# Kernel tuning notes

Measured on AMD Instinct MI355X. Metric: run time of the kernel, lower is better.

## Reference

```python
import jax, jax.numpy as jnp
import numpy as np

N = 100000   # num_nodes
E = 1600000  # num_edges
R = 8        # num_rels
B = 4        # num_bases
D = 64       # inp_dim = h_dim = out_dim


def setup_inputs() -> dict:
    key = jax.random.key(0)
    ks = jax.random.split(key, 16)
    s = 1.0 / np.sqrt(D)
    inp = {
        'h': jax.random.normal(ks[0], (N, D), jnp.float32),
        'src': jax.random.randint(ks[1], (E,), 0, N),
        'dst': jax.random.randint(ks[2], (E,), 0, N),
        'etype': jax.random.randint(ks[3], (E,), 0, R),
        'norm': jax.random.uniform(ks[4], (E, 1), jnp.float32),
    }
    for i in range(3):  # i2h, hidden, h2o layers (basis decomposition)
        inp[f'bases{i}'] = jax.random.normal(ks[5 + 2 * i], (B, D, D), jnp.float32) * s
        inp[f'wcomp{i}'] = jax.random.normal(ks[6 + 2 * i], (R, B), jnp.float32) * s
    inp['dec_w1'] = jax.random.normal(ks[11], (D, D), jnp.float32) * s
    inp['dec_b1'] = jnp.zeros((D,), jnp.float32)
    inp['dec_w2'] = jax.random.normal(ks[12], (D, 1), jnp.float32) * s
    inp['dec_b2'] = jnp.zeros((1,), jnp.float32)
    return inp


def rgcn_layer(h, src, dst, etype, norm, bases, wcomp, activate):
    # basis decomposition: W_r = sum_b wcomp[r,b] * bases[b]
    W = jnp.einsum('rb,bio->rio', wcomp, bases)           # [R, D, D]
    # transform all nodes under every relation (dense GEMM), then gather per edge
    Ht = jnp.einsum('ni,rio->rno', h, W).reshape(R * N, -1)  # [R*N, D]
    msg = Ht[etype * N + src] * norm                      # [E, D] gather + norm
    out = jax.ops.segment_sum(msg, dst, num_segments=N)   # scatter-add to dst
    return jax.nn.relu(out) if activate else out


def reference(h, src, dst, etype, norm, bases0, wcomp0, bases1, wcomp1,
              bases2, wcomp2, dec_w1, dec_b1, dec_w2, dec_b2):
    # EncoderRGCN: i2h (relu) -> hidden (relu) -> h2o (no activation)
    h1 = rgcn_layer(h, src, dst, etype, norm, bases0, wcomp0, True)
    h2 = rgcn_layer(h1, src, dst, etype, norm, bases1, wcomp1, True)
    henc = rgcn_layer(h2, src, dst, etype, norm, bases2, wcomp2, False)
    # AttributeDecoder: Linear -> ReLU -> Linear(reconstruct_dim=1)
    d1 = jax.nn.relu(henc @ dec_w1 + dec_b1)
    rec = (d1 @ dec_w2 + dec_b2).squeeze()                # [N]
    return rec, henc
```

## Files before the change

kernel.cpp:

```cpp
#include <hip/hip_runtime.h>

typedef _Float16 half8 __attribute__((ext_vector_type(8)));
typedef _Float16 half4 __attribute__((ext_vector_type(4)));
typedef _Float16 half2v __attribute__((ext_vector_type(2)));
typedef float floatx4 __attribute__((ext_vector_type(4)));

constexpr int NN = 100000;
constexpr int EE = 1600000;
constexpr int NBK = 196;
constexpr int CHUNK = 3125;
constexpr int CAPB = 12288;
constexpr int NDCAP = 48;

__global__ __launch_bounds__(256) void k_part(const int* __restrict__ dst,
                                              const int* __restrict__ src,
                                              const int* __restrict__ etype,
                                              const float* __restrict__ norm,
                                              int* __restrict__ gcur,
                                              int2* __restrict__ part) {
  __shared__ int2 ldata[CHUNK];
  __shared__ unsigned char lbkt[CHUNK];
  __shared__ int lhist[NBK], lbase[NBK + 1], lcur[NBK], gbase[NBK];
  __shared__ int sh[256];
  const int tid = threadIdx.x;
  const int e0 = blockIdx.x * CHUNK;

  for (int b = tid; b < NBK; b += 256) lhist[b] = 0;
  __syncthreads();
  for (int i = tid; i < CHUNK; i += 256)
    atomicAdd(&lhist[dst[e0 + i] >> 9], 1);
  __syncthreads();
  {
    const int v = (tid < NBK) ? lhist[tid] : 0;
    sh[tid] = v;
    __syncthreads();
    int run = v;
    for (int d = 1; d < 256; d <<= 1) {
      int t = (tid >= d) ? sh[tid - d] : 0;
      __syncthreads();
      run += t;
      sh[tid] = run;
      __syncthreads();
    }
    if (tid < NBK) {
      lbase[tid] = run - v;
      lcur[tid] = 0;
      gbase[tid] = tid * CAPB + atomicAdd(&gcur[tid], v);
    }
    if (tid == 0) lbase[NBK] = CHUNK;
  }
  __syncthreads();
  for (int i = tid; i < CHUNK; i += 256) {
    const int e = e0 + i;
    const int d = dst[e], s = src[e], et = etype[e];
    const _Float16 nh = (_Float16)norm[e];
    const unsigned short n16 = __builtin_bit_cast(unsigned short, nh);
    const int bk = d >> 9;
    const int pos = lbase[bk] + atomicAdd(&lcur[bk], 1);
    ldata[pos] = make_int2((d << 15) | (s >> 2), (s & 3) | (et << 2) | ((int)n16 << 5));
    lbkt[pos] = (unsigned char)bk;
  }
  __syncthreads();
  for (int i = tid; i < CHUNK; i += 256) {
    const int bk = (int)lbkt[i];
    part[gbase[bk] + (i - lbase[bk])] = ldata[i];
  }
}

__global__ __launch_bounds__(512) void k_part2(const int* __restrict__ gcur,
                                               const int2* __restrict__ part,
                                               int* __restrict__ off,
                                               int2* __restrict__ em) {
  __shared__ int hcnt[512];
  __shared__ int wred[8];
  __shared__ int swsum[8];
  const int tid = threadIdx.x;
  const int bk = blockIdx.x;
  const int nb0 = bk << 9;
  const int2* __restrict__ pp = part + (size_t)bk * CAPB;

  {
    int pv = (tid < bk) ? gcur[tid] : 0;
    for (int d = 32; d > 0; d >>= 1) pv += __shfl_down(pv, d);
    if ((tid & 63) == 0) wred[tid >> 6] = pv;
  }
  hcnt[tid] = 0;
  __syncthreads();
  int base = 0;
#pragma unroll
  for (int w = 0; w < 8; ++w) base += wred[w];
  const int cntb = gcur[bk];

  for (int i = tid; i < cntb; i += 512)
    atomicAdd(&hcnt[(((unsigned)pp[i].x) >> 15) & 511], 1);
  __syncthreads();
  const int v = hcnt[tid];
  int incl = v;
  for (int d = 1; d < 64; d <<= 1) {
    const int t = __shfl_up(incl, d);
    if ((tid & 63) >= d) incl += t;
  }
  if ((tid & 63) == 63) swsum[tid >> 6] = incl;
  __syncthreads();
  int pre = 0;
  for (int w = 0; w < (tid >> 6); ++w) pre += swsum[w];
  const int excl = pre + incl - v;
  {
    const int n = nb0 + tid;
    if (n < NN) off[n] = base + excl;
  }
  if (bk == NBK - 1 && tid == 0) off[NN] = EE;
  hcnt[tid] = excl;
  __syncthreads();
  for (int i = tid; i < cntb; i += 512) {
    const int2 r = pp[i];
    const int d = ((unsigned)r.x) >> 15;
    const int s = ((r.x & 0x7FFF) << 2) | (r.y & 3);
    const int et = (r.y >> 2) & 7;
    const unsigned short n16 = (unsigned short)((r.y >> 5) & 0xFFFF);
    const float nf = (float)__builtin_bit_cast(_Float16, n16);
    const int pos = atomicAdd(&hcnt[d & 511], 1);
    em[base + pos] = make_int2(((d & 15) << 23) | (et << 20) | s, __float_as_int(nf));
  }
}


__global__ __launch_bounds__(256) void k_prep(const float* __restrict__ h,
                                              _Float16* __restrict__ hh,
                                              const float* __restrict__ b0,
                                              const float* __restrict__ b1,
                                              const float* __restrict__ b2,
                                              _Float16* __restrict__ bbt,
                                              int* __restrict__ gcur) {
  const int bx = blockIdx.x;
  if (bx == 0 && threadIdx.x < NBK) gcur[threadIdx.x] = 0;
  if (bx < 6250) {
    const int i = bx * 256 + threadIdx.x;
    const float4 v = *(const float4*)&h[(size_t)i * 4];
    half4 o = {(_Float16)v.x, (_Float16)v.y, (_Float16)v.z, (_Float16)v.w};
    *(half4*)&hh[(size_t)i * 4] = o;
  } else {
    const int g = (bx - 6250) >> 6;
    const int idx = ((bx - 6250) & 63) * 256 + threadIdx.x;
    const float* bases = (g == 0) ? b0 : (g == 1) ? b1 : b2;
    const int o = idx >> 8, k = idx & 255;
    const int b = k >> 6, i = k & 63;
    bbt[g * 16384 + idx] = (_Float16)bases[b * 4096 + i * 64 + o];
  }
}

__global__ __launch_bounds__(256, 8) void k_layer(const _Float16* __restrict__ hh,
                                                  const int* __restrict__ off,
                                                  const int2* __restrict__ em,
                                                  const float* __restrict__ wcomp,
                                                  const _Float16* __restrict__ bbt,
                                                  _Float16* __restrict__ out16,
                                                  float* __restrict__ out32) {
  __shared__ _Float16 Ash[16 * 264];
  __shared__ int  ems_s[16 * NDCAP];
  __shared__ int2 ems_c[16 * NDCAP];
  __shared__ float4 wcs[8];
  __shared__ int offs[17];
  __shared__ int ovf;
  const int tid = threadIdx.x;
  const int lane = tid & 63;
  const int wv = tid >> 6;
  const int n0 = blockIdx.x * 16;

  if (tid < 17) offs[tid] = off[n0 + tid];
  if (tid == 0) ovf = 0;
  if (tid < 8) wcs[tid] = ((const float4*)wcomp)[tid];
  {
    const int4 z4 = make_int4(0, 0, 0, 0);
    int4* zs = (int4*)ems_s;
    int4* zc = (int4*)ems_c;
    if (tid < 192) zs[tid] = z4;
    for (int i = tid; i < 384; i += 256) zc[i] = z4;
  }
  __syncthreads();

  const int e0 = offs[0];
  const int len = offs[16] - e0;
  for (int i = tid; i < len; i += 256) {
    const int g = e0 + i;
    const int2 r = em[g];
    const int lo = (r.x >> 23) & 15;
    const int rank = g - offs[lo];
    const int et = (r.x >> 20) & 7;
    const int s = r.x & 0xFFFFF;
    const float nf = __int_as_float(r.y);
    const float4 w = wcs[et];
    const _Float16 c0 = (_Float16)(nf * w.x), c1 = (_Float16)(nf * w.y);
    const _Float16 c2 = (_Float16)(nf * w.z), c3 = (_Float16)(nf * w.w);
    const half2v p01 = {c0, c1}, p23 = {c2, c3};
    if (rank < NDCAP) {
      ems_s[lo * NDCAP + rank] = s;
      ems_c[lo * NDCAP + rank] = make_int2(
          __builtin_bit_cast(int, p01), __builtin_bit_cast(int, p23));
    } else ovf = 1;
  }
  __syncthreads();

#define LOADB(mm, bb, hv)                                                      \
  {                                                                            \
    const int4* sp4_ = (const int4*)&ems_s[(mm) * NDCAP + (bb) * 16 + eg * 8]; \
    const int4 sa_ = sp4_[0], sb_ = sp4_[1];                                   \
    hv[0] = hp[(unsigned)sa_.x * 32u + fl];                                    \
    hv[1] = hp[(unsigned)sa_.y * 32u + fl];                                    \
    hv[2] = hp[(unsigned)sa_.z * 32u + fl];                                    \
    hv[3] = hp[(unsigned)sa_.w * 32u + fl];                                    \
    hv[4] = hp[(unsigned)sb_.x * 32u + fl];                                    \
    hv[5] = hp[(unsigned)sb_.y * 32u + fl];                                    \
    hv[6] = hp[(unsigned)sb_.z * 32u + fl];                                    \
    hv[7] = hp[(unsigned)sb_.w * 32u + fl];                                    \
  }

#define FMAQ(mm, bb, hv, aq)                                                   \
  {                                                                            \
    const int4* cp4_ = (const int4*)&ems_c[(mm) * NDCAP + (bb) * 16 + eg * 8]; \
    _Pragma("unroll")                                                          \
    for (int k_ = 0; k_ < 4; ++k_) {                                           \
      const int4 c_ = cp4_[k_];                                                \
      const half2v pa01_ = __builtin_bit_cast(half2v, c_.x);                   \
      const half2v pa23_ = __builtin_bit_cast(half2v, c_.y);                   \
      const half2v pb01_ = __builtin_bit_cast(half2v, c_.z);                   \
      const half2v pb23_ = __builtin_bit_cast(half2v, c_.w);                   \
      aq[0] = aq[0] + hv[2 * k_] * __builtin_shufflevector(pa01_, pa01_, 0, 0);\
      aq[1] = aq[1] + hv[2 * k_] * __builtin_shufflevector(pa01_, pa01_, 1, 1);\
      aq[2] = aq[2] + hv[2 * k_] * __builtin_shufflevector(pa23_, pa23_, 0, 0);\
      aq[3] = aq[3] + hv[2 * k_] * __builtin_shufflevector(pa23_, pa23_, 1, 1);\
      aq[0] = aq[0] + hv[2 * k_ + 1] * __builtin_shufflevector(pb01_, pb01_, 0, 0);\
      aq[1] = aq[1] + hv[2 * k_ + 1] * __builtin_shufflevector(pb01_, pb01_, 1, 1);\
      aq[2] = aq[2] + hv[2 * k_ + 1] * __builtin_shufflevector(pb23_, pb23_, 0, 0);\
      aq[3] = aq[3] + hv[2 * k_ + 1] * __builtin_shufflevector(pb23_, pb23_, 1, 1);\
    }                                                                          \
  }

  if (!ovf) {
    const int fl = lane & 31;
    const int eg = lane >> 5;
    const half2v* __restrict__ hp = (const half2v*)hh;
    const int mb = wv * 4;
    const int oA = offs[mb], oB = offs[mb + 1], oC = offs[mb + 2],
              oD = offs[mb + 3], oE = offs[mb + 4];
    const int c0n = oB - oA, c1n = oC - oB, c2n = oD - oC, c3n = oE - oD;
    const int nb0_ = (c0n > 0) ? ((c0n + 15) >> 4) : 1;
    const int nb1_ = (c1n > 0) ? ((c1n + 15) >> 4) : 1;
    const int nb2_ = (c2n > 0) ? ((c2n + 15) >> 4) : 1;
    const int nb3_ = (c3n > 0) ? ((c3n + 15) >> 4) : 1;

    half2v acc[4][4];
#pragma unroll
    for (int q = 0; q < 4; ++q)
#pragma unroll
      for (int i = 0; i < 4; ++i) acc[q][i] = half2v{0, 0};

    half2v hvA[8], hvB[8];
    LOADB(mb, 0, hvA);
#pragma unroll
    for (int q = 0; q < 4; ++q) {
      const int m = mb + q;
      const int nbq = (q == 0) ? nb0_ : (q == 1) ? nb1_ : (q == 2) ? nb2_ : nb3_;
      if (q < 3) {
        if (q & 1) LOADB(m + 1, 0, hvA) else LOADB(m + 1, 0, hvB)
      }
      if (q & 1) FMAQ(m, 0, hvB, acc[q]) else FMAQ(m, 0, hvA, acc[q])
      for (int b = 1; b < nbq; ++b) {
        if (q & 1) {
          LOADB(m, b, hvB) FMAQ(m, b, hvB, acc[q])
        } else {
          LOADB(m, b, hvA) FMAQ(m, b, hvA, acc[q])
        }
      }
    }
#pragma unroll
    for (int q = 0; q < 4; ++q) {
      const int m = mb + q;
#pragma unroll
      for (int i = 0; i < 4; ++i)
        acc[q][i] = acc[q][i] + __builtin_bit_cast(half2v,
            __shfl_xor(__builtin_bit_cast(int, acc[q][i]), 32));
      if (eg == 0) {
        _Float16* ar = &Ash[m * 264];
        *(half2v*)&ar[0 * 64 + 2 * fl] = acc[q][0];
        *(half2v*)&ar[1 * 64 + 2 * fl] = acc[q][1];
        *(half2v*)&ar[2 * 64 + 2 * fl] = acc[q][2];
        *(half2v*)&ar[3 * 64 + 2 * fl] = acc[q][3];
      }
    }
  } else {
    const _Float16* hl = hh + lane;
    for (int q = 0; q < 4; ++q) {
      const int m = wv * 4 + q;
      const int p0 = offs[m], p1 = offs[m + 1];
      float a0 = 0.f, a1 = 0.f, a2 = 0.f, a3 = 0.f;
      for (int p = p0; p < p1; p += 8) {
#pragma unroll
        for (int j = 0; j < 8; ++j) {
          const bool live = (p + j < p1);
          const int idx = live ? p + j : p1 - 1;
          const int2 mm = em[idx];
          const float hv = (float)hl[(size_t)(mm.x & 0xFFFFF) << 6];
          const float wn = live ? __int_as_float(mm.y) : 0.f;
          const float4 w = wcs[(mm.x >> 20) & 7];
          const float t = wn * hv;
          a0 = fmaf(t, w.x, a0); a1 = fmaf(t, w.y, a1);
          a2 = fmaf(t, w.z, a2); a3 = fmaf(t, w.w, a3);
        }
      }
      _Float16* ar = &Ash[m * 264];
      ar[lane]       = (_Float16)a0;
      ar[64 + lane]  = (_Float16)a1;
      ar[128 + lane] = (_Float16)a2;
      ar[192 + lane] = (_Float16)a3;
    }
  }
  __syncthreads();

  const int col = lane & 15;
  const int quad = lane >> 4;
  const int obase = wv * 16 + col;
  const _Float16* ap = &Ash[col * 264 + quad * 8];
  const _Float16* bp = &bbt[(size_t)obase * 256 + quad * 8];
  floatx4 acc2 = {0.f, 0.f, 0.f, 0.f};
#pragma unroll
  for (int s = 0; s < 8; ++s) {
    const half8 af = *(const half8*)(ap + s * 32);
    const half8 bf = *(const half8*)(bp + s * 32);
    acc2 = __builtin_amdgcn_mfma_f32_16x16x32_f16(af, bf, acc2, 0, 0, 0);
  }
  if (out16) {
#pragma unroll
    for (int r = 0; r < 4; ++r) {
      const float c = fmaxf(acc2[r], 0.f);
      out16[(size_t)(n0 + quad * 4 + r) * 64 + obase] = (_Float16)c;
    }
  } else {
#pragma unroll
    for (int r = 0; r < 4; ++r) {
      out32[(size_t)(n0 + quad * 4 + r) * 64 + obase] = acc2[r];
    }
  }
#undef LOADB
#undef FMAQ
}

__global__ __launch_bounds__(256) void k_dec(const float* __restrict__ henc,
                                             const float* __restrict__ w1,
                                             const float* __restrict__ b1,
                                             const float* __restrict__ w2,
                                             const float* __restrict__ b2,
                                             float* __restrict__ rec) {
  __shared__ float w1s[64 * 64];
  __shared__ float hs[16 * 68];
  const int tid = threadIdx.x;
  for (int r = tid; r < 1024; r += 256)
    *(float4*)&w1s[r * 4] = *(const float4*)&w1[r * 4];
  const int og = tid & 15;
  const int nl = tid >> 4;
  const float4 wv2 = *(const float4*)&w2[og * 4];
  const float4 bv1 = *(const float4*)&b1[og * 4];
  const float b2v = b2[0];
  for (int t0 = blockIdx.x * 16; t0 < NN; t0 += gridDim.x * 16) {
    __syncthreads();
    {
      const float4 hv = *(const float4*)&henc[(size_t)t0 * 64 + tid * 4];
      *(float4*)&hs[(tid >> 4) * 68 + (tid & 15) * 4] = hv;
    }
    __syncthreads();
    float4 acc = bv1;
    const float* hr = &hs[nl * 68];
#pragma unroll 8
    for (int i = 0; i < 64; ++i) {
      const float hv = hr[i];
      const float4 wv = *(const float4*)&w1s[i * 64 + og * 4];
      acc.x = fmaf(hv, wv.x, acc.x); acc.y = fmaf(hv, wv.y, acc.y);
      acc.z = fmaf(hv, wv.z, acc.z); acc.w = fmaf(hv, wv.w, acc.w);
    }
    acc.x = fmaxf(acc.x, 0.f); acc.y = fmaxf(acc.y, 0.f);
    acc.z = fmaxf(acc.z, 0.f); acc.w = fmaxf(acc.w, 0.f);
    float v = acc.x * wv2.x + acc.y * wv2.y + acc.z * wv2.z + acc.w * wv2.w;
    v += __shfl_xor(v, 1); v += __shfl_xor(v, 2);
    v += __shfl_xor(v, 4); v += __shfl_xor(v, 8);
    if (og == 0) rec[t0 + nl] = v + b2v;
  }
}


extern "C" void kernel_launch(void* const* d_in, const int* in_sizes, int n_in,
                              void* d_out, int out_size, void* d_ws, size_t ws_size,
                              hipStream_t stream) {
  const float* h     = (const float*)d_in[0];
  const int*   src   = (const int*)d_in[1];
  const int*   dst   = (const int*)d_in[2];
  const int*   etype = (const int*)d_in[3];
  const float* norm  = (const float*)d_in[4];
  const float* bases[3] = {(const float*)d_in[5], (const float*)d_in[7], (const float*)d_in[9]};
  const float* wcomp[3] = {(const float*)d_in[6], (const float*)d_in[8], (const float*)d_in[10]};
  const float* dw1 = (const float*)d_in[11];
  const float* db1 = (const float*)d_in[12];
  const float* dw2 = (const float*)d_in[13];
  const float* db2 = (const float*)d_in[14];

  float* rec  = (float*)d_out;
  float* henc = (float*)d_out + NN;

  char* ws = (char*)d_ws;
  int*      off    = (int*)(ws + 0);
  int*      gcur   = (int*)(ws + 400512);
  int2*     em     = (int2*)(ws + 402560);
  _Float16* hh     = (_Float16*)(ws + 13202560);
  _Float16* h1f    = (_Float16*)(ws + 26002560);
  _Float16* h2f    = (_Float16*)(ws + 38802560);
  _Float16* bbt    = (_Float16*)(ws + 51602560);
  int2*     part   = (int2*)h1f;

  k_prep<<<6250 + 192, 256, 0, stream>>>(h, hh, bases[0], bases[1], bases[2], bbt, gcur);

  k_part<<<512, 256, 0, stream>>>(dst, src, etype, norm, gcur, part);
  k_part2<<<NBK, 512, 0, stream>>>(gcur, part, off, em);

  k_layer<<<NN / 16, 256, 0, stream>>>(hh,  off, em, wcomp[0], bbt,         h1f, nullptr);
  k_layer<<<NN / 16, 256, 0, stream>>>(h1f, off, em, wcomp[1], bbt + 16384, h2f, nullptr);
  k_layer<<<NN / 16, 256, 0, stream>>>(h2f, off, em, wcomp[2], bbt + 32768, nullptr, henc);

  k_dec<<<256, 256, 0, stream>>>(henc, dw1, db1, dw2, db2, rec);
}
```

Measured before the change: 350.2 us.

## Software-pipeline layer gather with triple buffers and widen partition and decoder launches

In the layer kernel's non-overflow path, the per-node loop over 16-edge batches becomes a fully unrolled, interleaved schedule with three rotating register buffers. It covers at most three batches per node, with loads for later nodes issued ahead of the multiply-adds for earlier ones, to hide gather latency. Separately, the two partition kernels move to 512 and 1024 threads per block, with guards added to the scan and histogram code, and the decoder grid grows from 256 to 1024 blocks. The unrolled schedule uses more registers, which may lower occupancy.

Measured after the change: 896.6 us. 156% more time.

```diff
diff --git a/kernel.cpp b/kernel.cpp
--- a/kernel.cpp
+++ b/kernel.cpp
@@ -12,7 +12,7 @@
 constexpr int CAPB = 12288;
 constexpr int NDCAP = 48;
 
-__global__ __launch_bounds__(256) void k_part(const int* __restrict__ dst,
+__global__ __launch_bounds__(512) void k_part(const int* __restrict__ dst,
                                               const int* __restrict__ src,
                                               const int* __restrict__ etype,
                                               const float* __restrict__ norm,
@@ -25,21 +25,21 @@
   const int tid = threadIdx.x;
   const int e0 = blockIdx.x * CHUNK;
 
-  for (int b = tid; b < NBK; b += 256) lhist[b] = 0;
-  __syncthreads();
-  for (int i = tid; i < CHUNK; i += 256)
+  if (tid < NBK) lhist[tid] = 0;
+  __syncthreads();
+  for (int i = tid; i < CHUNK; i += 512)
     atomicAdd(&lhist[dst[e0 + i] >> 9], 1);
   __syncthreads();
   {
     const int v = (tid < NBK) ? lhist[tid] : 0;
-    sh[tid] = v;
+    if (tid < 256) sh[tid] = v;
     __syncthreads();
     int run = v;
     for (int d = 1; d < 256; d <<= 1) {
-      int t = (tid >= d) ? sh[tid - d] : 0;
+      const int t = (tid >= d && tid < 256) ? sh[tid - d] : 0;
       __syncthreads();
       run += t;
-      sh[tid] = run;
+      if (tid < 256) sh[tid] = run;
       __syncthreads();
     }
     if (tid < NBK) {
@@ -50,7 +50,7 @@
     if (tid == 0) lbase[NBK] = CHUNK;
   }
   __syncthreads();
-  for (int i = tid; i < CHUNK; i += 256) {
+  for (int i = tid; i < CHUNK; i += 512) {
     const int e = e0 + i;
     const int d = dst[e], s = src[e], et = etype[e];
     const _Float16 nh = (_Float16)norm[e];
@@ -61,18 +61,18 @@
     lbkt[pos] = (unsigned char)bk;
   }
   __syncthreads();
-  for (int i = tid; i < CHUNK; i += 256) {
+  for (int i = tid; i < CHUNK; i += 512) {
     const int bk = (int)lbkt[i];
     part[gbase[bk] + (i - lbase[bk])] = ldata[i];
   }
 }
 
-__global__ __launch_bounds__(512) void k_part2(const int* __restrict__ gcur,
-                                               const int2* __restrict__ part,
-                                               int* __restrict__ off,
-                                               int2* __restrict__ em) {
+__global__ __launch_bounds__(1024) void k_part2(const int* __restrict__ gcur,
+                                                const int2* __restrict__ part,
+                                                int* __restrict__ off,
+                                                int2* __restrict__ em) {
   __shared__ int hcnt[512];
-  __shared__ int wred[8];
+  __shared__ int wred[16];
   __shared__ int swsum[8];
   const int tid = threadIdx.x;
   const int bk = blockIdx.x;
@@ -84,35 +84,35 @@
     for (int d = 32; d > 0; d >>= 1) pv += __shfl_down(pv, d);
     if ((tid & 63) == 0) wred[tid >> 6] = pv;
   }
-  hcnt[tid] = 0;
+  if (tid < 512) hcnt[tid] = 0;
   __syncthreads();
   int base = 0;
 #pragma unroll
-  for (int w = 0; w < 8; ++w) base += wred[w];
+  for (int w = 0; w < 16; ++w) base += wred[w];
   const int cntb = gcur[bk];
 
-  for (int i = tid; i < cntb; i += 512)
+  for (int i = tid; i < cntb; i += 1024)
     atomicAdd(&hcnt[(((unsigned)pp[i].x) >> 15) & 511], 1);
   __syncthreads();
-  const int v = hcnt[tid];
+  const int v = (tid < 512) ? hcnt[tid] : 0;
   int incl = v;
   for (int d = 1; d < 64; d <<= 1) {
     const int t = __shfl_up(incl, d);
     if ((tid & 63) >= d) incl += t;
   }
-  if ((tid & 63) == 63) swsum[tid >> 6] = incl;
-  __syncthreads();
-  int pre = 0;
-  for (int w = 0; w < (tid >> 6); ++w) pre += swsum[w];
-  const int excl = pre + incl - v;
-  {
+  if (tid < 512 && (tid & 63) == 63) swsum[tid >> 6] = incl;
+  __syncthreads();
+  if (tid < 512) {
+    int pre = 0;
+    for (int w = 0; w < (tid >> 6); ++w) pre += swsum[w];
+    const int excl = pre + incl - v;
     const int n = nb0 + tid;
     if (n < NN) off[n] = base + excl;
+    hcnt[tid] = excl;
   }
   if (bk == NBK - 1 && tid == 0) off[NN] = EE;
-  hcnt[tid] = excl;
-  __syncthreads();
-  for (int i = tid; i < cntb; i += 512) {
+  __syncthreads();
+  for (int i = tid; i < cntb; i += 1024) {
     const int2 r = pp[i];
     const int d = ((unsigned)r.x) >> 15;
     const int s = ((r.x & 0x7FFF) << 2) | (r.y & 3);
@@ -244,10 +244,8 @@
     const int oA = offs[mb], oB = offs[mb + 1], oC = offs[mb + 2],
               oD = offs[mb + 3], oE = offs[mb + 4];
     const int c0n = oB - oA, c1n = oC - oB, c2n = oD - oC, c3n = oE - oD;
-    const int nb0_ = (c0n > 0) ? ((c0n + 15) >> 4) : 1;
-    const int nb1_ = (c1n > 0) ? ((c1n + 15) >> 4) : 1;
-    const int nb2_ = (c2n > 0) ? ((c2n + 15) >> 4) : 1;
-    const int nb3_ = (c3n > 0) ? ((c3n + 15) >> 4) : 1;
+    const bool v1_0 = c0n > 16, v1_1 = c1n > 16, v1_2 = c2n > 16, v1_3 = c3n > 16;
+    const bool v2_0 = c0n > 32, v2_1 = c1n > 32, v2_2 = c2n > 32, v2_3 = c3n > 32;
 
     half2v acc[4][4];
 #pragma unroll
@@ -255,24 +253,32 @@
 #pragma unroll
       for (int i = 0; i < 4; ++i) acc[q][i] = half2v{0, 0};
 
-    half2v hvA[8], hvB[8];
-    LOADB(mb, 0, hvA);
-#pragma unroll
-    for (int q = 0; q < 4; ++q) {
-      const int m = mb + q;
-      const int nbq = (q == 0) ? nb0_ : (q == 1) ? nb1_ : (q == 2) ? nb2_ : nb3_;
-      if (q < 3) {
-        if (q & 1) LOADB(m + 1, 0, hvA) else LOADB(m + 1, 0, hvB)
-      }
-      if (q & 1) FMAQ(m, 0, hvB, acc[q]) else FMAQ(m, 0, hvA, acc[q])
-      for (int b = 1; b < nbq; ++b) {
-        if (q & 1) {
-          LOADB(m, b, hvB) FMAQ(m, b, hvB, acc[q])
-        } else {
-          LOADB(m, b, hvA) FMAQ(m, b, hvA, acc[q])
-        }
-      }
-    }
+    half2v bA[8], bB[8], bC[8];
+    LOADB(mb + 0, 0, bA)
+    LOADB(mb + 1, 0, bB)
+    LOADB(mb + 2, 0, bC)
+    FMAQ(mb + 0, 0, bA, acc[0])
+    LOADB(mb + 3, 0, bA)
+    FMAQ(mb + 1, 0, bB, acc[1])
+    if (v1_0) LOADB(mb + 0, 1, bB)
+    FMAQ(mb + 2, 0, bC, acc[2])
+    if (v1_1) LOADB(mb + 1, 1, bC)
+    FMAQ(mb + 3, 0, bA, acc[3])
+    if (v1_2) LOADB(mb + 2, 1, bA)
+    if (v1_0) { FMAQ(mb + 0, 1, bB, acc[0]) }
+    if (v1_3) LOADB(mb + 3, 1, bB)
+    if (v1_1) { FMAQ(mb + 1, 1, bC, acc[1]) }
+    if (v2_0) LOADB(mb + 0, 2, bC)
+    if (v1_2) { FMAQ(mb + 2, 1, bA, acc[2]) }
+    if (v2_1) LOADB(mb + 1, 2, bA)
+    if (v1_3) { FMAQ(mb + 3, 1, bB, acc[3]) }
+    if (v2_2) LOADB(mb + 2, 2, bB)
+    if (v2_0) { FMAQ(mb + 0, 2, bC, acc[0]) }
+    if (v2_3) LOADB(mb + 3, 2, bC)
+    if (v2_1) { FMAQ(mb + 1, 2, bA, acc[1]) }
+    if (v2_2) { FMAQ(mb + 2, 2, bB, acc[2]) }
+    if (v2_3) { FMAQ(mb + 3, 2, bC, acc[3]) }
+
 #pragma unroll
     for (int q = 0; q < 4; ++q) {
       const int m = mb + q;
@@ -417,12 +423,12 @@
 
   k_prep<<<6250 + 192, 256, 0, stream>>>(h, hh, bases[0], bases[1], bases[2], bbt, gcur);
 
-  k_part<<<512, 256, 0, stream>>>(dst, src, etype, norm, gcur, part);
-  k_part2<<<NBK, 512, 0, stream>>>(gcur, part, off, em);
+  k_part<<<512, 512, 0, stream>>>(dst, src, etype, norm, gcur, part);
+  k_part2<<<NBK, 1024, 0, stream>>>(gcur, part, off, em);
 
   k_layer<<<NN / 16, 256, 0, stream>>>(hh,  off, em, wcomp[0], bbt,         h1f, nullptr);
   k_layer<<<NN / 16, 256, 0, stream>>>(h1f, off, em, wcomp[1], bbt + 16384, h2f, nullptr);
   k_layer<<<NN / 16, 256, 0, stream>>>(h2f, off, em, wcomp[2], bbt + 32768, nullptr, henc);
 
-  k_dec<<<256, 256, 0, stream>>>(henc, dw1, db1, dw2, db2, rec);
-}
+  k_dec<<<1024, 256, 0, stream>>>(henc, dw1, db1, dw2, db2, rec);
+}
```
